# Optimization experiments

Hardware: AMD Instinct MI355X
Metric: run time of the kernel (lower is better)

Reference implementation:

```python
import jax, jax.numpy as jnp
import numpy as np


def setup_inputs() -> dict:
    key = jax.random.key(0)
    k_x, k_w1, k_w2 = jax.random.split(key, 3)
    B, N, F, H = 32, 1024, 512, 2048
    x = jax.random.normal(k_x, (B, N, F), dtype=jnp.float32)
    # first: orthogonal-ish init (Gaussian is fine as a stand-in for correctness testing)
    W1 = jax.random.normal(k_w1, (H, F), dtype=jnp.float32) / np.sqrt(F)
    b1 = jnp.zeros((H,), dtype=jnp.float32)
    # second: normal(std=0.01)
    W2 = jax.random.normal(k_w2, (F, H), dtype=jnp.float32) * 0.01
    b2 = jnp.zeros((F,), dtype=jnp.float32)
    return {"x": x, "W1": W1, "b1": b1, "W2": W2, "b2": b2, "dim": 1}


def reference(x, W1, b1, W2, b2, dim):
    # Move the target feature axis (1 + dim) to last position.
    x = jnp.moveaxis(x, 1 + dim, -1)  # [B, N, F]
    srt = jnp.argsort(x, axis=-1)     # argsort indices
    inv = jnp.argsort(srt, axis=-1)   # inverse permutation
    # torch: x.scatter(-1, argsort, x) -> out[argsort[i]] = x[i] == gather by inverse
    xs = jnp.take_along_axis(x, inv, axis=-1)
    # 2-layer MLP with skip
    h = jax.nn.relu(jnp.einsum('bnf,hf->bnh', xs, W1) + b1)
    y = jnp.einsum('bnh,fh->bnf', h, W2) + b2 + xs
    # torch: y.scatter(-1, inverse, y) -> out[inverse[i]] = y[i] == gather by argsort
    out = jnp.take_along_axis(y, srt, axis=-1)
    return jnp.moveaxis(out, -1, 1 + dim)
```

## Files before the change

### kernel.cpp

```cpp
#include <hip/hip_runtime.h>
#include <hip/hip_bf16.h>

typedef __hip_bfloat16 bf16;
typedef __attribute__((ext_vector_type(8))) short bf16x8;
typedef __attribute__((ext_vector_type(4))) float f32x4;

#define ASYNC_CP16(gsrc, ldst)                                                              \
  __builtin_amdgcn_global_load_lds(                                                         \
      (const __attribute__((address_space(1))) unsigned int*)(gsrc),                        \
      (__attribute__((address_space(3))) unsigned int*)(ldst), 16, 0, 0)

#define BB 32
#define NN 1024
#define FF 512
#define HH 2048
#define M_ROWS (BB * NN)

__global__ __launch_bounds__(256) void cvt_pair(const float* __restrict__ a, bf16* __restrict__ da,
                                                const float* __restrict__ b, bf16* __restrict__ db,
                                                int n) {
  int i = blockIdx.x * 256 + threadIdx.x;
  if (i < n) {
    da[i] = __float2bfloat16(a[i]);
    db[i] = __float2bfloat16(b[i]);
  }
}

template <int IMM>
__device__ __forceinline__ unsigned long long swz64(unsigned long long k) {
  int lo = __builtin_amdgcn_ds_swizzle((int)(unsigned)k, IMM);
  int hi = __builtin_amdgcn_ds_swizzle((int)(unsigned)(k >> 32), IMM);
  return (((unsigned long long)(unsigned)hi) << 32) | (unsigned)lo;
}

__global__ __launch_bounds__(256) void sort_rows_wave(const float* __restrict__ x,
                                                      unsigned* __restrict__ xs_pack,
                                                      unsigned* __restrict__ srt_pack) {
  __shared__ __align__(16) unsigned short scatx[4 * FF];
  const int t = threadIdx.x;
  const int lane = t & 63;
  const int w = t >> 6;
  const size_t row = (size_t)blockIdx.x * 4 + w;
  const float* xr = x + row * FF;

  float4 v0 = *(const float4*)(xr + lane * 8);
  float4 v1 = *(const float4*)(xr + lane * 8 + 4);
  float vals[8] = {v0.x, v0.y, v0.z, v0.w, v1.x, v1.y, v1.z, v1.w};

  unsigned long long key[8];
#pragma unroll
  for (int r = 0; r < 8; r++) {
    unsigned u = __float_as_uint(vals[r]);
    unsigned s = u ^ ((unsigned)((int)u >> 31) | 0x80000000u);
    key[r] = ((unsigned long long)s << 32) | (unsigned)(lane * 8 + r);
  }

#pragma unroll
  for (int k = 2; k <= 512; k <<= 1) {
#pragma unroll
    for (int j = k >> 1; j > 0; j >>= 1) {
      if (j >= 8) {
        const int d = j >> 3;
        unsigned long long o[8];
#pragma unroll
        for (int r = 0; r < 8; r++) {
          if (d == 1)       o[r] = swz64<0x041F>(key[r]);
          else if (d == 2)  o[r] = swz64<0x081F>(key[r]);
          else if (d == 4)  o[r] = swz64<0x101F>(key[r]);
          else if (d == 8)  o[r] = swz64<0x201F>(key[r]);
          else if (d == 16) o[r] = swz64<0x401F>(key[r]);
          else              o[r] = __shfl_xor(key[r], 32, 64);
        }
        bool asc = (((lane * 8) & k) == 0);
        bool lower = ((lane & d) == 0);
        bool keep = (asc == lower);
#pragma unroll
        for (int r = 0; r < 8; r++) {
          bool mine = key[r] < o[r];
          key[r] = (mine == keep) ? key[r] : o[r];
        }
      } else {
#pragma unroll
        for (int r = 0; r < 8; r++) {
          if ((r & j) == 0) {
            const int a = r, b = r | j;
            bool asc = (((lane * 8 + a) & k) == 0);
            unsigned long long ka = key[a], kb = key[b];
            bool sw = ((ka > kb) == asc);
            key[a] = sw ? kb : ka;
            key[b] = sw ? ka : kb;
          }
        }
      }
    }
  }

  const int base = w * FF;
  unsigned j8[8];
#pragma unroll
  for (int r = 0; r < 8; r++) {
    j8[r] = (unsigned)key[r] & 0xFFFFu;
    __hip_bfloat16 hb = __float2bfloat16(vals[r]);
    scatx[base + j8[r]] = *(unsigned short*)&hb;
  }

  uint4 so;
  so.x = j8[0] | (j8[1] << 16);
  so.y = j8[2] | (j8[3] << 16);
  so.z = j8[4] | (j8[5] << 16);
  so.w = j8[6] | (j8[7] << 16);
  *(uint4*)(srt_pack + row * 256 + lane * 4) = so;

  __syncthreads();
  uint4 xo = *(const uint4*)&scatx[base + lane * 8];
  *(uint4*)(xs_pack + row * 256 + lane * 4) = xo;
}

template <int RELU, int ADDX, int K, int N>
__global__ __launch_bounds__(512, 2) void gemm8p(const bf16* __restrict__ A,
                                                 const bf16* __restrict__ Bw,
                                                 const float* __restrict__ bias,
                                                 const bf16* __restrict__ xs_add,
                                                 bf16* __restrict__ C) {
  __shared__ __align__(16) bf16 S[65536];
  const int t = threadIdx.x;
  const int lane = t & 63, wave = t >> 6;
  const int waveM = wave >> 2, waveN = wave & 3;
  const size_t mBase = (size_t)blockIdx.x * 256;
  const size_t nBase = (size_t)blockIdx.y * 256;

  const int srow = t >> 2;
  const int sclog = (t & 3) ^ ((t >> 3) & 3);
  const bf16* Asrc0 = A + (mBase + srow) * (size_t)K + sclog * 8;
  const bf16* Bsrc0 = Bw + (nBase + srow) * (size_t)K + sclog * 8;
  const int sdA = wave * 512;
  const int sdB = 32768 + wave * 512;

  const int fr = lane & 15;
  const int swz8 = ((lane >> 4) ^ ((lane >> 1) & 3)) * 8;
  const int aRd = (waveM * 128 + fr) * 32 + swz8;
  const int bRd = 32768 + (waveN * 64 + fr) * 32 + swz8;

#define STAGE_A(tt, ks)                                           \
  do {                                                            \
    const int rb_ = (((tt) & 1) * 2 + (ks)) * 8192 + sdA;         \
    const bf16* g_ = Asrc0 + (size_t)(tt) * 64 + (ks) * 32;       \
    ASYNC_CP16(g_, &S[rb_]);                                      \
    ASYNC_CP16(g_ + (size_t)128 * K, &S[rb_ + 4096]);             \
  } while (0)
#define STAGE_B(tt, ks)                                           \
  do {                                                            \
    const int rb_ = (((tt) & 1) * 2 + (ks)) * 8192 + sdB;         \
    const bf16* g_ = Bsrc0 + (size_t)(tt) * 64 + (ks) * 32;       \
    ASYNC_CP16(g_, &S[rb_]);                                      \
    ASYNC_CP16(g_ + (size_t)128 * K, &S[rb_ + 4096]);             \
  } while (0)

  f32x4 acc[8][4];
  f32x4 zero = {0.f, 0.f, 0.f, 0.f};
#pragma unroll
  for (int i = 0; i < 8; i++)
#pragma unroll
    for (int j = 0; j < 4; j++) acc[i][j] = zero;

  STAGE_A(0, 0);
  STAGE_B(0, 0);
  STAGE_A(0, 1);
  STAGE_B(0, 1);
  asm volatile("s_waitcnt vmcnt(4)" ::: "memory");
  __builtin_amdgcn_s_barrier();

  const int NT = K / 64;
  for (int kt = 0; kt < NT; ++kt) {
    const int buf = kt & 1;
    const bool pf = (kt + 1 < NT);
    bf16x8 af[4], bq[4];

    {
      const int rg = buf * 16384;
#pragma unroll
      for (int i = 0; i < 4; i++) af[i] = *(const bf16x8*)&S[rg + aRd + i * 512];
#pragma unroll
      for (int n = 0; n < 4; n++) bq[n] = *(const bf16x8*)&S[rg + bRd + n * 512];
      if (pf) STAGE_A(kt + 1, 0);
      __builtin_amdgcn_s_barrier();
      asm volatile("s_waitcnt lgkmcnt(0)" ::: "memory");
      __builtin_amdgcn_sched_barrier(0);
      __builtin_amdgcn_s_setprio(1);
#pragma unroll
      for (int i = 0; i < 4; i++)
#pragma unroll
        for (int n = 0; n < 4; n++)
          acc[i][n] = __builtin_amdgcn_mfma_f32_16x16x32_bf16(af[i], bq[n], acc[i][n], 0, 0, 0);
      __builtin_amdgcn_s_setprio(0);
      __builtin_amdgcn_s_barrier();
    }
    {
      const int rg = buf * 16384;
#pragma unroll
      for (int i = 0; i < 4; i++) af[i] = *(const bf16x8*)&S[rg + aRd + 2048 + i * 512];
      if (pf) STAGE_B(kt + 1, 0);
      __builtin_amdgcn_s_barrier();
      asm volatile("s_waitcnt lgkmcnt(0)" ::: "memory");
      __builtin_amdgcn_sched_barrier(0);
      __builtin_amdgcn_s_setprio(1);
#pragma unroll
      for (int i = 0; i < 4; i++)
#pragma unroll
        for (int n = 0; n < 4; n++)
          acc[4 + i][n] = __builtin_amdgcn_mfma_f32_16x16x32_bf16(af[i], bq[n], acc[4 + i][n], 0, 0, 0);
      __builtin_amdgcn_s_setprio(0);
      if (pf) asm volatile("s_waitcnt vmcnt(4)" ::: "memory");
      else    asm volatile("s_waitcnt vmcnt(0)" ::: "memory");
      __builtin_amdgcn_s_barrier();
    }
    {
      const int rg = buf * 16384 + 8192;
#pragma unroll
      for (int i = 0; i < 4; i++) af[i] = *(const bf16x8*)&S[rg + aRd + i * 512];
#pragma unroll
      for (int n = 0; n < 4; n++) bq[n] = *(const bf16x8*)&S[rg + bRd + n * 512];
      if (pf) STAGE_A(kt + 1, 1);
      __builtin_amdgcn_s_barrier();
      asm volatile("s_waitcnt lgkmcnt(0)" ::: "memory");
      __builtin_amdgcn_sched_barrier(0);
      __builtin_amdgcn_s_setprio(1);
#pragma unroll
      for (int i = 0; i < 4; i++)
#pragma unroll
        for (int n = 0; n < 4; n++)
          acc[i][n] = __builtin_amdgcn_mfma_f32_16x16x32_bf16(af[i], bq[n], acc[i][n], 0, 0, 0);
      __builtin_amdgcn_s_setprio(0);
      __builtin_amdgcn_s_barrier();
    }
    {
      const int rg = buf * 16384 + 8192;
#pragma unroll
      for (int i = 0; i < 4; i++) af[i] = *(const bf16x8*)&S[rg + aRd + 2048 + i * 512];
      if (pf) STAGE_B(kt + 1, 1);
      __builtin_amdgcn_s_barrier();
      asm volatile("s_waitcnt lgkmcnt(0)" ::: "memory");
      __builtin_amdgcn_sched_barrier(0);
      __builtin_amdgcn_s_setprio(1);
#pragma unroll
      for (int i = 0; i < 4; i++)
#pragma unroll
        for (int n = 0; n < 4; n++)
          acc[4 + i][n] = __builtin_amdgcn_mfma_f32_16x16x32_bf16(af[i], bq[n], acc[4 + i][n], 0, 0, 0);
      __builtin_amdgcn_s_setprio(0);
      if (pf) asm volatile("s_waitcnt vmcnt(4)" ::: "memory");
      __builtin_amdgcn_s_barrier();
    }
  }
#undef STAGE_A
#undef STAGE_B

  const int cn = lane & 15;
  const int cm = (lane >> 4) * 4;
  float b4[4];
#pragma unroll
  for (int n = 0; n < 4; n++) b4[n] = bias[nBase + waveN * 64 + n * 16 + cn];
#pragma unroll
  for (int mt = 0; mt < 8; mt++) {
#pragma unroll
    for (int n = 0; n < 4; n++) {
      size_t gn = nBase + waveN * 64 + n * 16 + cn;
#pragma unroll
      for (int r = 0; r < 4; r++) {
        size_t gm = mBase + waveM * 128 + mt * 16 + cm + r;
        float v = acc[mt][n][r] + b4[n];
        if (RELU) v = fmaxf(v, 0.f);
        if (ADDX) v += __bfloat162float(xs_add[gm * (size_t)N + gn]);
        C[gm * (size_t)N + gn] = __float2bfloat16(v);
      }
    }
  }
}

__global__ __launch_bounds__(256) void permute_gather(const bf16* __restrict__ zp,
                                                      const unsigned* __restrict__ srt_pack,
                                                      float* __restrict__ out) {
  __shared__ __align__(16) unsigned short zr[4][FF];
  const int t = threadIdx.x;
  const int lane = t & 63;
  const int w = t >> 6;
  const size_t row = (size_t)blockIdx.x * 4 + w;

  *(uint4*)&zr[w][lane * 8] = *(const uint4*)(zp + row * FF + lane * 8);
  uint4 sv = *(const uint4*)(srt_pack + row * 256 + lane * 4);
  __syncthreads();

  unsigned idx[8] = {sv.x & 0xFFFFu, sv.x >> 16, sv.y & 0xFFFFu, sv.y >> 16,
                     sv.z & 0xFFFFu, sv.z >> 16, sv.w & 0xFFFFu, sv.w >> 16};
  float4 o0, o1;
#pragma unroll
  for (int r = 0; r < 8; r++) {
    float zf = __uint_as_float(((unsigned)zr[w][idx[r]]) << 16);
    ((r < 4) ? (&o0.x) : (&o1.x))[r & 3] = zf;
  }
  *(float4*)(out + row * FF + lane * 8) = o0;
  *(float4*)(out + row * FF + lane * 8 + 4) = o1;
}

extern "C" void kernel_launch(void* const* d_in, const int* in_sizes, int n_in,
                              void* d_out, int out_size, void* d_ws, size_t ws_size,
                              hipStream_t stream) {
  const float* x  = (const float*)d_in[0];
  const float* W1 = (const float*)d_in[1];
  const float* b1 = (const float*)d_in[2];
  const float* W2 = (const float*)d_in[3];
  const float* b2 = (const float*)d_in[4];
  float* out = (float*)d_out;

  char* ws = (char*)d_ws;
  unsigned* xs  = (unsigned*)(ws);
  bf16*     xsb = (bf16*)(ws);
  bf16*     z   = (bf16*)(ws);
  unsigned* srt = (unsigned*)(ws + 33554432);
  bf16* h   = (bf16*)(ws + 67108864);
  bf16* W1b = (bf16*)(ws + 201326592);
  bf16* W2b = (bf16*)(ws + 203423744);

  cvt_pair<<<(HH * FF + 255) / 256, 256, 0, stream>>>(W1, W1b, W2, W2b, HH * FF);
  sort_rows_wave<<<M_ROWS / 4, 256, 0, stream>>>(x, xs, srt);
  gemm8p<1, 0, FF, HH><<<dim3(M_ROWS / 256, HH / 256), 512, 0, stream>>>(xsb, W1b, b1, nullptr, h);
  gemm8p<0, 1, HH, FF><<<dim3(M_ROWS / 256, FF / 256), 512, 0, stream>>>(h, W2b, b2, xsb, z);
  permute_gather<<<M_ROWS / 4, 256, 0, stream>>>(z, srt, out);
}
```

Before: 348.6 us.

## Fuse both MLP GEMMs into one kernel keeping hidden activations in LDS

```diff
diff --git a/kernel.cpp b/kernel.cpp
--- a/kernel.cpp
+++ b/kernel.cpp
@@ -116,162 +116,200 @@
   *(uint4*)(xs_pack + row * 256 + lane * 4) = xo;
 }
 
-template <int RELU, int ADDX, int K, int N>
-__global__ __launch_bounds__(512, 2) void gemm8p(const bf16* __restrict__ A,
-                                                 const bf16* __restrict__ Bw,
-                                                 const float* __restrict__ bias,
-                                                 const bf16* __restrict__ xs_add,
-                                                 bf16* __restrict__ C) {
-  __shared__ __align__(16) bf16 S[65536];
+__global__ __launch_bounds__(512, 2) void fused_mlp(const bf16* __restrict__ xsb,
+                                                    const bf16* __restrict__ W1b,
+                                                    const float* __restrict__ b1,
+                                                    const bf16* __restrict__ W2b,
+                                                    const float* __restrict__ b2,
+                                                    bf16* __restrict__ Z) {
+  __shared__ __align__(16) unsigned char S[163840];
+  const int XSO = 0;
+  const int W1O = 32768;
+  const int W2O = 65536;
+  const int HOF = 131072;
+
   const int t = threadIdx.x;
   const int lane = t & 63, wave = t >> 6;
   const int waveM = wave >> 2, waveN = wave & 3;
-  const size_t mBase = (size_t)blockIdx.x * 256;
-  const size_t nBase = (size_t)blockIdx.y * 256;
-
-  const int srow = t >> 2;
-  const int sclog = (t & 3) ^ ((t >> 3) & 3);
-  const bf16* Asrc0 = A + (mBase + srow) * (size_t)K + sclog * 8;
-  const bf16* Bsrc0 = Bw + (nBase + srow) * (size_t)K + sclog * 8;
-  const int sdA = wave * 512;
-  const int sdB = 32768 + wave * 512;
-
-  const int fr = lane & 15;
-  const int swz8 = ((lane >> 4) ^ ((lane >> 1) & 3)) * 8;
-  const int aRd = (waveM * 128 + fr) * 32 + swz8;
-  const int bRd = 32768 + (waveN * 64 + fr) * 32 + swz8;
-
-#define STAGE_A(tt, ks)                                           \
-  do {                                                            \
-    const int rb_ = (((tt) & 1) * 2 + (ks)) * 8192 + sdA;         \
-    const bf16* g_ = Asrc0 + (size_t)(tt) * 64 + (ks) * 32;       \
-    ASYNC_CP16(g_, &S[rb_]);                                      \
-    ASYNC_CP16(g_ + (size_t)128 * K, &S[rb_ + 4096]);             \
+  const int fr = lane & 15, q = lane >> 4;
+  const int m0 = (int)blockIdx.x * 128;
+
+  const int r64 = t >> 3;
+  const int sl3 = (t & 7) ^ (r64 & 7);
+  const bf16* xsg0 = xsb + (size_t)(m0 + r64) * FF + sl3 * 8;
+  const bf16* w1g0 = W1b + (size_t)r64 * FF + sl3 * 8;
+  const int r32 = t >> 2;
+  const int sl2 = (t & 3) ^ ((t >> 3) & 3);
+  const bf16* w2g0 = W2b + (size_t)r32 * HH + sl2 * 8;
+
+#define STAGE_XS(kc_)                                                        \
+  do {                                                                       \
+    const int d_ = XSO + ((kc_) & 1) * 16384 + t * 16;                       \
+    const bf16* g_ = xsg0 + (kc_) * 64;                                      \
+    ASYNC_CP16(g_, &S[d_]);                                                  \
+    ASYNC_CP16(g_ + (size_t)64 * FF, &S[d_ + 8192]);                         \
   } while (0)
-#define STAGE_B(tt, ks)                                           \
-  do {                                                            \
-    const int rb_ = (((tt) & 1) * 2 + (ks)) * 8192 + sdB;         \
-    const bf16* g_ = Bsrc0 + (size_t)(tt) * 64 + (ks) * 32;       \
-    ASYNC_CP16(g_, &S[rb_]);                                      \
-    ASYNC_CP16(g_ + (size_t)128 * K, &S[rb_ + 4096]);             \
+#define STAGE_W1(ht_, kc_)                                                   \
+  do {                                                                       \
+    const int d_ = W1O + ((kc_) & 1) * 16384 + t * 16;                       \
+    const bf16* g_ = w1g0 + (size_t)(ht_) * 128 * FF + (kc_) * 64;           \
+    ASYNC_CP16(g_, &S[d_]);                                                  \
+    ASYNC_CP16(g_ + (size_t)64 * FF, &S[d_ + 8192]);                         \
   } while (0)
-
-  f32x4 acc[8][4];
+#define STAGE_W2(ht_, zc_)                                                   \
+  do {                                                                       \
+    const int d_ = W2O + ((zc_) & 1) * 32768 + t * 16;                       \
+    const bf16* g_ = w2g0 + (ht_) * 128 + (zc_) * 32;                        \
+    ASYNC_CP16(g_, &S[d_]);                                                  \
+    ASYNC_CP16(g_ + (size_t)128 * HH, &S[d_ + 8192]);                        \
+    ASYNC_CP16(g_ + (size_t)256 * HH, &S[d_ + 16384]);                       \
+    ASYNC_CP16(g_ + (size_t)384 * HH, &S[d_ + 24576]);                       \
+  } while (0)
+
   f32x4 zero = {0.f, 0.f, 0.f, 0.f};
-#pragma unroll
-  for (int i = 0; i < 8; i++)
-#pragma unroll
-    for (int j = 0; j < 4; j++) acc[i][j] = zero;
-
-  STAGE_A(0, 0);
-  STAGE_B(0, 0);
-  STAGE_A(0, 1);
-  STAGE_B(0, 1);
-  asm volatile("s_waitcnt vmcnt(4)" ::: "memory");
+  f32x4 za[4][8];
+  f32x4 ha[4][2];
+#pragma unroll
+  for (int i = 0; i < 4; i++)
+#pragma unroll
+    for (int j = 0; j < 8; j++) za[i][j] = zero;
+#pragma unroll
+  for (int i = 0; i < 4; i++)
+#pragma unroll
+    for (int j = 0; j < 2; j++) ha[i][j] = zero;
+
+  STAGE_XS(0);
+  STAGE_W1(0, 0);
+  asm volatile("s_waitcnt vmcnt(0)" ::: "memory");
   __builtin_amdgcn_s_barrier();
 
-  const int NT = K / 64;
-  for (int kt = 0; kt < NT; ++kt) {
-    const int buf = kt & 1;
-    const bool pf = (kt + 1 < NT);
-    bf16x8 af[4], bq[4];
-
-    {
-      const int rg = buf * 16384;
-#pragma unroll
-      for (int i = 0; i < 4; i++) af[i] = *(const bf16x8*)&S[rg + aRd + i * 512];
-#pragma unroll
-      for (int n = 0; n < 4; n++) bq[n] = *(const bf16x8*)&S[rg + bRd + n * 512];
-      if (pf) STAGE_A(kt + 1, 0);
+  for (int ht = 0; ht < 16; ++ht) {
+    for (int kc = 0; kc < 8; ++kc) {
+      const int xo = XSO + (kc & 1) * 16384;
+      const int wo = W1O + (kc & 1) * 16384;
+      bf16x8 aw[2][2], bx[2][4];
+#pragma unroll
+      for (int ks = 0; ks < 2; ks++) {
+#pragma unroll
+        for (int Ht = 0; Ht < 2; Ht++) {
+          const int row = waveN * 32 + Ht * 16 + fr;
+          aw[ks][Ht] = *(const bf16x8*)&S[wo + row * 128 + (((ks * 4 + q) ^ (row & 7)) * 16)];
+        }
+#pragma unroll
+        for (int Mt = 0; Mt < 4; Mt++) {
+          const int row = waveM * 64 + Mt * 16 + fr;
+          bx[ks][Mt] = *(const bf16x8*)&S[xo + row * 128 + (((ks * 4 + q) ^ (row & 7)) * 16)];
+        }
+      }
+      if (kc < 7) {
+        STAGE_XS(kc + 1);
+        STAGE_W1(ht, kc + 1);
+      }
+      if (kc == 6) STAGE_W2(ht, 0);
       __builtin_amdgcn_s_barrier();
       asm volatile("s_waitcnt lgkmcnt(0)" ::: "memory");
       __builtin_amdgcn_sched_barrier(0);
       __builtin_amdgcn_s_setprio(1);
 #pragma unroll
-      for (int i = 0; i < 4; i++)
-#pragma unroll
-        for (int n = 0; n < 4; n++)
-          acc[i][n] = __builtin_amdgcn_mfma_f32_16x16x32_bf16(af[i], bq[n], acc[i][n], 0, 0, 0);
+      for (int ks = 0; ks < 2; ks++)
+#pragma unroll
+        for (int Mt = 0; Mt < 4; Mt++)
+#pragma unroll
+          for (int Ht = 0; Ht < 2; Ht++)
+            ha[Mt][Ht] = __builtin_amdgcn_mfma_f32_16x16x32_bf16(aw[ks][Ht], bx[ks][Mt],
+                                                                 ha[Mt][Ht], 0, 0, 0);
       __builtin_amdgcn_s_setprio(0);
-      __builtin_amdgcn_s_barrier();
-    }
+      if (kc == 6) asm volatile("s_waitcnt vmcnt(4)" ::: "memory");
+      else         asm volatile("s_waitcnt vmcnt(0)" ::: "memory");
+      __builtin_amdgcn_s_barrier();
+    }
+
     {
-      const int rg = buf * 16384;
-#pragma unroll
-      for (int i = 0; i < 4; i++) af[i] = *(const bf16x8*)&S[rg + aRd + 2048 + i * 512];
-      if (pf) STAGE_B(kt + 1, 0);
+      float b1v[8];
+#pragma unroll
+      for (int Ht = 0; Ht < 2; Ht++)
+#pragma unroll
+        for (int r = 0; r < 4; r++)
+          b1v[Ht * 4 + r] = b1[ht * 128 + waveN * 32 + Ht * 16 + q * 4 + r];
+#pragma unroll
+      for (int Mt = 0; Mt < 4; Mt++) {
+        const int M = waveM * 64 + Mt * 16 + fr;
+        const int mb = HOF + M * 256;
+        const int key = M & 7;
+#pragma unroll
+        for (int Ht = 0; Ht < 2; Ht++) {
+          const int Hb = waveN * 32 + Ht * 16 + q * 4;
+          const int slot = Hb >> 3;
+          const int inslot = (Hb * 2) & 15;
+          float v0 = fmaxf(ha[Mt][Ht][0] + b1v[Ht * 4 + 0], 0.f);
+          float v1 = fmaxf(ha[Mt][Ht][1] + b1v[Ht * 4 + 1], 0.f);
+          float v2 = fmaxf(ha[Mt][Ht][2] + b1v[Ht * 4 + 2], 0.f);
+          float v3 = fmaxf(ha[Mt][Ht][3] + b1v[Ht * 4 + 3], 0.f);
+          __hip_bfloat16 h0 = __float2bfloat16(v0), h1 = __float2bfloat16(v1);
+          __hip_bfloat16 h2 = __float2bfloat16(v2), h3 = __float2bfloat16(v3);
+          uint2 pk;
+          pk.x = (unsigned)*(unsigned short*)&h0 | ((unsigned)*(unsigned short*)&h1 << 16);
+          pk.y = (unsigned)*(unsigned short*)&h2 | ((unsigned)*(unsigned short*)&h3 << 16);
+          *(uint2*)&S[mb + ((slot ^ key) * 16) + inslot] = pk;
+          ha[Mt][Ht] = zero;
+        }
+      }
+      asm volatile("s_waitcnt lgkmcnt(0)" ::: "memory");
+      __builtin_amdgcn_s_barrier();
+    }
+
+    for (int zc = 0; zc < 4; ++zc) {
+      const int zo = W2O + (zc & 1) * 32768;
+      bf16x8 ah[4], bw[8];
+#pragma unroll
+      for (int Mt = 0; Mt < 4; Mt++) {
+        const int M = waveM * 64 + Mt * 16 + fr;
+        ah[Mt] = *(const bf16x8*)&S[HOF + M * 256 + (((zc * 4 + q) ^ (M & 7)) * 16)];
+      }
+#pragma unroll
+      for (int Ft = 0; Ft < 8; Ft++) {
+        const int row = waveN * 128 + Ft * 16 + fr;
+        bw[Ft] = *(const bf16x8*)&S[zo + row * 64 + ((q ^ ((row >> 1) & 3)) * 16)];
+      }
+      if (zc < 3) {
+        STAGE_W2(ht, zc + 1);
+      } else if (ht < 15) {
+        STAGE_XS(0);
+        STAGE_W1(ht + 1, 0);
+      }
       __builtin_amdgcn_s_barrier();
       asm volatile("s_waitcnt lgkmcnt(0)" ::: "memory");
       __builtin_amdgcn_sched_barrier(0);
       __builtin_amdgcn_s_setprio(1);
 #pragma unroll
-      for (int i = 0; i < 4; i++)
-#pragma unroll
-        for (int n = 0; n < 4; n++)
-          acc[4 + i][n] = __builtin_amdgcn_mfma_f32_16x16x32_bf16(af[i], bq[n], acc[4 + i][n], 0, 0, 0);
+      for (int Mt = 0; Mt < 4; Mt++)
+#pragma unroll
+        for (int Ft = 0; Ft < 8; Ft++)
+          za[Mt][Ft] = __builtin_amdgcn_mfma_f32_16x16x32_bf16(ah[Mt], bw[Ft], za[Mt][Ft], 0, 0, 0);
       __builtin_amdgcn_s_setprio(0);
-      if (pf) asm volatile("s_waitcnt vmcnt(4)" ::: "memory");
-      else    asm volatile("s_waitcnt vmcnt(0)" ::: "memory");
-      __builtin_amdgcn_s_barrier();
-    }
-    {
-      const int rg = buf * 16384 + 8192;
-#pragma unroll
-      for (int i = 0; i < 4; i++) af[i] = *(const bf16x8*)&S[rg + aRd + i * 512];
-#pragma unroll
-      for (int n = 0; n < 4; n++) bq[n] = *(const bf16x8*)&S[rg + bRd + n * 512];
-      if (pf) STAGE_A(kt + 1, 1);
-      __builtin_amdgcn_s_barrier();
-      asm volatile("s_waitcnt lgkmcnt(0)" ::: "memory");
-      __builtin_amdgcn_sched_barrier(0);
-      __builtin_amdgcn_s_setprio(1);
-#pragma unroll
-      for (int i = 0; i < 4; i++)
-#pragma unroll
-        for (int n = 0; n < 4; n++)
-          acc[i][n] = __builtin_amdgcn_mfma_f32_16x16x32_bf16(af[i], bq[n], acc[i][n], 0, 0, 0);
-      __builtin_amdgcn_s_setprio(0);
-      __builtin_amdgcn_s_barrier();
-    }
-    {
-      const int rg = buf * 16384 + 8192;
-#pragma unroll
-      for (int i = 0; i < 4; i++) af[i] = *(const bf16x8*)&S[rg + aRd + 2048 + i * 512];
-      if (pf) STAGE_B(kt + 1, 1);
-      __builtin_amdgcn_s_barrier();
-      asm volatile("s_waitcnt lgkmcnt(0)" ::: "memory");
-      __builtin_amdgcn_sched_barrier(0);
-      __builtin_amdgcn_s_setprio(1);
-#pragma unroll
-      for (int i = 0; i < 4; i++)
-#pragma unroll
-        for (int n = 0; n < 4; n++)
-          acc[4 + i][n] = __builtin_amdgcn_mfma_f32_16x16x32_bf16(af[i], bq[n], acc[4 + i][n], 0, 0, 0);
-      __builtin_amdgcn_s_setprio(0);
-      if (pf) asm volatile("s_waitcnt vmcnt(4)" ::: "memory");
-      __builtin_amdgcn_s_barrier();
-    }
-  }
-#undef STAGE_A
-#undef STAGE_B
-
-  const int cn = lane & 15;
-  const int cm = (lane >> 4) * 4;
-  float b4[4];
-#pragma unroll
-  for (int n = 0; n < 4; n++) b4[n] = bias[nBase + waveN * 64 + n * 16 + cn];
-#pragma unroll
-  for (int mt = 0; mt < 8; mt++) {
-#pragma unroll
-    for (int n = 0; n < 4; n++) {
-      size_t gn = nBase + waveN * 64 + n * 16 + cn;
+      asm volatile("s_waitcnt vmcnt(0)" ::: "memory");
+      __builtin_amdgcn_s_barrier();
+    }
+  }
+#undef STAGE_XS
+#undef STAGE_W1
+#undef STAGE_W2
+
+  const int cn = fr;
+  const int cm = q * 4;
+  float bz[8];
+#pragma unroll
+  for (int Ft = 0; Ft < 8; Ft++) bz[Ft] = b2[waveN * 128 + Ft * 16 + cn];
+#pragma unroll
+  for (int Mt = 0; Mt < 4; Mt++) {
+#pragma unroll
+    for (int Ft = 0; Ft < 8; Ft++) {
+      const size_t gn = waveN * 128 + Ft * 16 + cn;
 #pragma unroll
       for (int r = 0; r < 4; r++) {
-        size_t gm = mBase + waveM * 128 + mt * 16 + cm + r;
-        float v = acc[mt][n][r] + b4[n];
-        if (RELU) v = fmaxf(v, 0.f);
-        if (ADDX) v += __bfloat162float(xs_add[gm * (size_t)N + gn]);
-        C[gm * (size_t)N + gn] = __float2bfloat16(v);
+        const size_t gm = m0 + waveM * 64 + Mt * 16 + cm + r;
+        float v = za[Mt][Ft][r] + bz[Ft] + __bfloat162float(xsb[gm * FF + gn]);
+        Z[gm * FF + gn] = __float2bfloat16(v);
       }
     }
   }
@@ -315,15 +353,13 @@
   char* ws = (char*)d_ws;
   unsigned* xs  = (unsigned*)(ws);
   bf16*     xsb = (bf16*)(ws);
-  bf16*     z   = (bf16*)(ws);
   unsigned* srt = (unsigned*)(ws + 33554432);
-  bf16* h   = (bf16*)(ws + 67108864);
-  bf16* W1b = (bf16*)(ws + 201326592);
-  bf16* W2b = (bf16*)(ws + 203423744);
+  bf16* z   = (bf16*)(ws + 67108864);
+  bf16* W1b = (bf16*)(ws + 100663296);
+  bf16* W2b = (bf16*)(ws + 102760448);
 
   cvt_pair<<<(HH * FF + 255) / 256, 256, 0, stream>>>(W1, W1b, W2, W2b, HH * FF);
   sort_rows_wave<<<M_ROWS / 4, 256, 0, stream>>>(x, xs, srt);
-  gemm8p<1, 0, FF, HH><<<dim3(M_ROWS / 256, HH / 256), 512, 0, stream>>>(xsb, W1b, b1, nullptr, h);
-  gemm8p<0, 1, HH, FF><<<dim3(M_ROWS / 256, FF / 256), 512, 0, stream>>>(h, W2b, b2, xsb, z);
+  fused_mlp<<<M_ROWS / 128, 512, 0, stream>>>(xsb, W1b, b1, W2b, b2, z);
   permute_gather<<<M_ROWS / 4, 256, 0, stream>>>(z, srt, out);
 }
```

New measurement: 637.8 us. +83.0%, slower.
